# Optimization experiments

Measured on AMD Instinct MI355X. Metric: run time of the kernel, lower is better.

Reference implementation:

```python
import jax, jax.numpy as jnp
import numpy as np


def gcn_conv(x, src, dst, deg_inv_sqrt, W, b, n_nodes):
    # PyG GCNConv: linear transform first, then normalized aggregation (A_hat = D^-1/2 (A+I) D^-1/2)
    h = x @ W                                   # [N, out]
    norm = deg_inv_sqrt[src] * deg_inv_sqrt[dst]  # [E+N]
    msg = h[src] * norm[:, None]                # gather + scale
    out = jax.ops.segment_sum(msg, dst, num_segments=n_nodes)
    return out + b


def setup_inputs() -> dict:
    key = jax.random.key(0)
    ks = jax.random.split(key, 10)
    N, E, D_in, D_h = 50000, 640000, 128, 64
    x = jax.random.normal(ks[0], (N, D_in), dtype=jnp.float32)
    edge_index = jax.random.randint(ks[1], (2, E), 0, N, dtype=jnp.int64)

    def glorot(k, fan_in, fan_out):
        lim = jnp.sqrt(6.0 / (fan_in + fan_out)).astype(jnp.float32)
        return jax.random.uniform(k, (fan_in, fan_out), jnp.float32, -lim, lim)

    return {
        "x": x,
        "edge_index": edge_index,
        "W1": glorot(ks[2], D_in, D_h), "b1": jnp.zeros((D_h,), jnp.float32),
        "W2": glorot(ks[3], D_h, D_h),  "b2": jnp.zeros((D_h,), jnp.float32),
        "W3": glorot(ks[4], D_h, D_h),  "b3": jnp.zeros((D_h,), jnp.float32),
        "W4": glorot(ks[5], D_h, D_in), "b4": jnp.zeros((D_in,), jnp.float32),
    }


def reference(x, edge_index, W1, b1, W2, b2, W3, b3, W4, b4):
    n = x.shape[0]
    loops = jnp.arange(n, dtype=edge_index.dtype)
    src = jnp.concatenate([edge_index[0], loops])  # A + I self-loops
    dst = jnp.concatenate([edge_index[1], loops])
    deg = jax.ops.segment_sum(jnp.ones_like(dst, dtype=x.dtype), dst, num_segments=n)
    deg_inv_sqrt = jnp.where(deg > 0, jax.lax.rsqrt(deg), 0.0)

    h = jax.nn.relu(gcn_conv(x, src, dst, deg_inv_sqrt, W1, b1, n))
    # dropout is identity in eval mode
    z = jax.nn.relu(gcn_conv(h, src, dst, deg_inv_sqrt, W2, b2, n))
    x_hat = jax.nn.relu(gcn_conv(z, src, dst, deg_inv_sqrt, W3, b3, n))
    x_hat = gcn_conv(x_hat, src, dst, deg_inv_sqrt, W4, b4, n)
    return (x_hat, z)
```

## Files before the change

kernel.cpp:

```cpp
#include <hip/hip_runtime.h>
#include <hip/hip_bf16.h>



__global__ __launch_bounds__(256) void init_all(int4* __restrict__ ell4, int nEll4,
                                                int* __restrict__ deg,
                                                int* __restrict__ cursor, int N,
                                                unsigned* __restrict__ gAz,
                                                unsigned* __restrict__ gBz) {
    int i = blockIdx.x * 256 + threadIdx.x;
    if (i < nEll4) ell4[i] = make_int4(N, N, N, N);
    if (i < N) { deg[i] = 0; cursor[i] = 0; }
    if (i < 32) { gAz[i] = 0u; gBz[i] = 0u; }
}

__global__ __launch_bounds__(256) void hist_deg(const int* __restrict__ dst,
                                                int* __restrict__ deg, int E) {
    int e = blockIdx.x * 256 + threadIdx.x;
    if (e < E) atomicAdd(&deg[dst[e]], 1);
}

__global__ __launch_bounds__(256) void dis_k(const int* __restrict__ deg,
                                             float* __restrict__ dis, int N) {
    int i = blockIdx.x * 256 + threadIdx.x;
    if (i < N) dis[i] = rsqrtf((float)(deg[i] + 1));
}

__global__ __launch_bounds__(256) void fill_ell(const int* __restrict__ src,
                                                const int* __restrict__ dst,
                                                int* __restrict__ cursor,
                                                int* __restrict__ ell, int E) {
    int e = blockIdx.x * 256 + threadIdx.x;
    if (e < E) {
        int d = dst[e];
        int slot = atomicAdd(&cursor[d], 1);
        if (slot < 64) ell[(size_t)d * 64 + slot] = src[e];
    }
}


__device__ __forceinline__ ushort r16(float f) {
    __hip_bfloat16 h = __float2bfloat16(f);
    return *reinterpret_cast<ushort*>(&h);
}
__device__ __forceinline__ float bf_lo(unsigned u) {
    return __builtin_bit_cast(float, u << 16);
}
__device__ __forceinline__ float bf_hi(unsigned u) {
    return __builtin_bit_cast(float, u & 0xFFFF0000u);
}

__device__ __forceinline__ void gather_pair_ell(const unsigned* __restrict__ G,
                                                const int* __restrict__ ell,
                                                int n0, int n1c,
                                                int lenA, int lenB, int lane,
                                                float& s0o, float& s1o,
                                                float& s2o, float& s3o) {
    int l32 = lane & 31;
    int idxA = ell[(size_t)n0 * 64 + l32];
    int idxB = ell[(size_t)n1c * 64 + l32];

    int grp     = lane >> 4;
    int p       = grp & 1;
    int nodeSel = grp >> 1;
    int f       = lane & 15;

    int cA = lenA < 32 ? lenA : 32;
    int cB = lenB < 32 ? lenB : 32;
    int cM = cA > cB ? cA : cB;
    int pM = (cM + 1) >> 1;

    float a0 = 0.f, a1 = 0.f, a2 = 0.f, a3 = 0.f;
    float b0 = 0.f, b1 = 0.f, b2 = 0.f, b3 = 0.f;

    for (int k = 0; k < pM; k += 8) {
        uint2 u[8];
#pragma unroll
        for (int i = 0; i < 8; ++i) {
            int e = p + 2 * (k + i);
            int sA = __shfl(idxA, e);
            int sB = __shfl(idxB, e);
            int s = nodeSel ? sB : sA;
            u[i] = *reinterpret_cast<const uint2*>(G + (unsigned)s * 32u + 2 * f);
        }
#pragma unroll
        for (int i = 0; i < 8; ++i) {
            if (i & 1) {
                b0 += bf_lo(u[i].x); b1 += bf_hi(u[i].x);
                b2 += bf_lo(u[i].y); b3 += bf_hi(u[i].y);
            } else {
                a0 += bf_lo(u[i].x); a1 += bf_hi(u[i].x);
                a2 += bf_lo(u[i].y); a3 += bf_hi(u[i].y);
            }
        }
    }
    int nOwn   = nodeSel ? n1c : n0;
    int lenOwn = nodeSel ? lenB : lenA;
    if (lenOwn > 64) lenOwn = 64;
    for (int e2 = 32 + p; e2 < lenOwn; e2 += 2) {
        int s = ell[(size_t)nOwn * 64 + e2];
        uint2 v = *reinterpret_cast<const uint2*>(G + (unsigned)s * 32u + 2 * f);
        a0 += bf_lo(v.x); a1 += bf_hi(v.x);
        a2 += bf_lo(v.y); a3 += bf_hi(v.y);
    }

    float r0 = a0 + b0, r1 = a1 + b1, r2 = a2 + b2, r3 = a3 + b3;
    r0 += __shfl_xor(r0, 16);
    r1 += __shfl_xor(r1, 16);
    r2 += __shfl_xor(r2, 16);
    r3 += __shfl_xor(r3, 16);
    s0o = r0; s1o = r1; s2o = r2; s3o = r3;
}

template <int K, int DOUT>
__global__ __launch_bounds__(256) void gemm_scale(const float* __restrict__ A,
                                                  const float* __restrict__ W,
                                                  const float* __restrict__ dis,
                                                  ushort* __restrict__ G16, int N) {
    constexpr int CG   = DOUT / 4;
    constexpr int RG   = 256 / CG;
    constexpr int ROWS = RG * 4;
    constexpr int LDA  = K + 4;

    __shared__ __align__(16) float a_lds[ROWS * LDA];
    __shared__ __align__(16) float w_lds[K * DOUT];

    int t    = threadIdx.x;
    int row0 = blockIdx.x * ROWS;

    constexpr int WF4 = K * DOUT / 4;
    for (int q = t; q < WF4; q += 256)
        reinterpret_cast<float4*>(w_lds)[q] =
            reinterpret_cast<const float4*>(W)[q];

    constexpr int AF4 = ROWS * K / 4;
    for (int q = t; q < AF4; q += 256) {
        int r  = q / (K / 4);
        int kc = q % (K / 4);
        float4 v = make_float4(0.f, 0.f, 0.f, 0.f);
        int gr = row0 + r;
        if (gr < N)
            v = reinterpret_cast<const float4*>(A + (size_t)gr * K)[kc];
        *reinterpret_cast<float4*>(&a_lds[r * LDA + kc * 4]) = v;
    }
    __syncthreads();

    int c0 = (t % CG) * 4;
    int r0 = (t / CG) * 4;

    float4 acc[4] = {};
#pragma unroll 1
    for (int k = 0; k < K; k += 4) {
        float4 w0 = *reinterpret_cast<const float4*>(&w_lds[(k + 0) * DOUT + c0]);
        float4 w1 = *reinterpret_cast<const float4*>(&w_lds[(k + 1) * DOUT + c0]);
        float4 w2 = *reinterpret_cast<const float4*>(&w_lds[(k + 2) * DOUT + c0]);
        float4 w3 = *reinterpret_cast<const float4*>(&w_lds[(k + 3) * DOUT + c0]);
#pragma unroll
        for (int j = 0; j < 4; ++j) {
            float4 a4 = *reinterpret_cast<const float4*>(&a_lds[(r0 + j) * LDA + k]);
            acc[j].x += a4.x * w0.x + a4.y * w1.x + a4.z * w2.x + a4.w * w3.x;
            acc[j].y += a4.x * w0.y + a4.y * w1.y + a4.z * w2.y + a4.w * w3.y;
            acc[j].z += a4.x * w0.z + a4.y * w1.z + a4.z * w2.z + a4.w * w3.z;
            acc[j].w += a4.x * w0.w + a4.y * w1.w + a4.z * w2.w + a4.w * w3.w;
        }
    }

#pragma unroll
    for (int j = 0; j < 4; ++j) {
        int gr = row0 + r0 + j;
        if (gr < N) {
            float s = dis[gr];
            float4 o = acc[j];
            ushort4 pk;
            pk.x = r16(o.x * s); pk.y = r16(o.y * s);
            pk.z = r16(o.z * s); pk.w = r16(o.w * s);
            *reinterpret_cast<ushort4*>(&G16[(size_t)gr * DOUT + c0]) = pk;
        }
    }
}

template <int K, int DOUT>
__global__ __launch_bounds__(256) void gemm_bias(const float* __restrict__ A,
                                                 const float* __restrict__ W,
                                                 const float* __restrict__ bias,
                                                 float* __restrict__ Out, int N) {
    constexpr int CG   = DOUT / 4;
    constexpr int RG   = 256 / CG;
    constexpr int ROWS = RG * 4;
    constexpr int LDA  = K + 4;

    __shared__ __align__(16) float a_lds[ROWS * LDA];
    __shared__ __align__(16) float w_lds[K * DOUT];

    int t    = threadIdx.x;
    int row0 = blockIdx.x * ROWS;

    constexpr int WF4 = K * DOUT / 4;
    for (int q = t; q < WF4; q += 256)
        reinterpret_cast<float4*>(w_lds)[q] =
            reinterpret_cast<const float4*>(W)[q];

    constexpr int AF4 = ROWS * K / 4;
    for (int q = t; q < AF4; q += 256) {
        int r  = q / (K / 4);
        int kc = q % (K / 4);
        float4 v = make_float4(0.f, 0.f, 0.f, 0.f);
        int gr = row0 + r;
        if (gr < N)
            v = reinterpret_cast<const float4*>(A + (size_t)gr * K)[kc];
        *reinterpret_cast<float4*>(&a_lds[r * LDA + kc * 4]) = v;
    }
    __syncthreads();

    int c0 = (t % CG) * 4;
    int r0 = (t / CG) * 4;

    float4 acc[4] = {};
#pragma unroll 1
    for (int k = 0; k < K; k += 4) {
        float4 w0 = *reinterpret_cast<const float4*>(&w_lds[(k + 0) * DOUT + c0]);
        float4 w1 = *reinterpret_cast<const float4*>(&w_lds[(k + 1) * DOUT + c0]);
        float4 w2 = *reinterpret_cast<const float4*>(&w_lds[(k + 2) * DOUT + c0]);
        float4 w3 = *reinterpret_cast<const float4*>(&w_lds[(k + 3) * DOUT + c0]);
#pragma unroll
        for (int j = 0; j < 4; ++j) {
            float4 a4 = *reinterpret_cast<const float4*>(&a_lds[(r0 + j) * LDA + k]);
            acc[j].x += a4.x * w0.x + a4.y * w1.x + a4.z * w2.x + a4.w * w3.x;
            acc[j].y += a4.x * w0.y + a4.y * w1.y + a4.z * w2.y + a4.w * w3.y;
            acc[j].z += a4.x * w0.z + a4.y * w1.z + a4.z * w2.z + a4.w * w3.z;
            acc[j].w += a4.x * w0.w + a4.y * w1.w + a4.z * w2.w + a4.w * w3.w;
        }
    }

    float4 b4v = *reinterpret_cast<const float4*>(&bias[c0]);
#pragma unroll
    for (int j = 0; j < 4; ++j) {
        int gr = row0 + r0 + j;
        if (gr < N) {
            float4 o = acc[j];
            o.x += b4v.x; o.y += b4v.y; o.z += b4v.z; o.w += b4v.w;
            reinterpret_cast<float4*>(Out + (size_t)gr * DOUT)[c0 / 4] = o;
        }
    }
}

template <bool WRITE_F32>
__global__ __launch_bounds__(256) void agg_gemm_pair(
    const unsigned* __restrict__ G,
    const int* __restrict__ deg,
    const int* __restrict__ ell,
    const float* __restrict__ dis,
    const float* __restrict__ bias,
    const float* __restrict__ Wn,
    unsigned* __restrict__ Gout,
    float* __restrict__ Zout,
    int N) {
    __shared__ __align__(16) float w_lds[64 * 64];
    __shared__ __align__(16) float a_buf[4][2][64];

    int t = threadIdx.x;
    for (int q = t; q < 64 * 64 / 4; q += 256)
        reinterpret_cast<float4*>(w_lds)[q] =
            reinterpret_cast<const float4*>(Wn)[q];
    __syncthreads();

    int wave = t >> 6, lane = t & 63;
    int h = lane >> 5, fl = lane & 31;
    int grp = lane >> 4, f = lane & 15;

    int n0 = (blockIdx.x * 4 + wave) * 2;
    if (n0 >= N) return;
    int n1 = n0 + 1;
    bool hasB = (n1 < N);
    int n1c = hasB ? n1 : n0;
    int nn = h ? n1c : n0;

    int lenA = deg[n0];
    int lenB = hasB ? deg[n1c] : 0;

    float dn0 = dis[n0], dn1 = dis[n1c];
    uint2 us2 = *reinterpret_cast<const uint2*>(G + (size_t)nn * 32 + 2 * f);
    float4 b4 = reinterpret_cast<const float4*>(bias)[f];

    float s0, s1, s2, s3;
    gather_pair_ell(G, ell, n0, n1c, lenA, lenB, lane, s0, s1, s2, s3);

    float dn = h ? dn1 : dn0;
    float v0 = fmaxf(dn * (s0 + bf_lo(us2.x)) + b4.x, 0.f);
    float v1 = fmaxf(dn * (s1 + bf_hi(us2.x)) + b4.y, 0.f);
    float v2 = fmaxf(dn * (s2 + bf_lo(us2.y)) + b4.z, 0.f);
    float v3 = fmaxf(dn * (s3 + bf_hi(us2.y)) + b4.w, 0.f);

    if ((grp & 1) == 0)
        *reinterpret_cast<float4*>(&a_buf[wave][h][4 * f]) =
            make_float4(v0, v1, v2, v3);
    if (WRITE_F32 && (grp == 0 || (grp == 2 && hasB)))
        *reinterpret_cast<float4*>(Zout + (size_t)nn * 64 + 4 * f) =
            make_float4(v0, v1, v2, v3);

    __builtin_amdgcn_wave_barrier();

    float yA0 = 0.f, yA1 = 0.f, yA2 = 0.f, yA3 = 0.f;
    float yB0 = 0.f, yB1 = 0.f, yB2 = 0.f, yB3 = 0.f;
    for (int k = 0; k < 64; k += 4) {
        float4 a4 = *reinterpret_cast<const float4*>(&a_buf[wave][0][k]);
        float4 c4 = *reinterpret_cast<const float4*>(&a_buf[wave][1][k]);
        float w0 = w_lds[(k + 0) * 64 + lane];
        float w1 = w_lds[(k + 1) * 64 + lane];
        float w2 = w_lds[(k + 2) * 64 + lane];
        float w3 = w_lds[(k + 3) * 64 + lane];
        yA0 += a4.x * w0; yA1 += a4.y * w1; yA2 += a4.z * w2; yA3 += a4.w * w3;
        yB0 += c4.x * w0; yB1 += c4.y * w1; yB2 += c4.z * w2; yB3 += c4.w * w3;
    }
    float yA = (yA0 + yA1) + (yA2 + yA3);
    float yB = (yB0 + yB1) + (yB2 + yB3);

    float l0 = __shfl(yA, 2 * fl), h0 = __shfl(yA, 2 * fl + 1);
    float l1 = __shfl(yB, 2 * fl), h1 = __shfl(yB, 2 * fl + 1);
    float yl = h ? l1 : l0;
    float yh = h ? h1 : h0;
    if (h == 0 || hasB) {
        unsigned pk = (unsigned)r16(dn * yl) | ((unsigned)r16(dn * yh) << 16);
        Gout[(unsigned)nn * 32u + fl] = pk;
    }
}

__global__ __launch_bounds__(256) void aggregate_s3(
    const unsigned* __restrict__ G,
    const int* __restrict__ deg,
    const int* __restrict__ ell,
    const float* __restrict__ dis,
    const float* __restrict__ bias,
    unsigned* __restrict__ Out, int N) {
    int t = threadIdx.x;
    int wave = t >> 6, lane = t & 63;
    int h = lane >> 5;
    int grp = lane >> 4, f = lane & 15;

    int n0 = (blockIdx.x * 4 + wave) * 2;
    if (n0 >= N) return;
    int n1 = n0 + 1;
    bool hasB = (n1 < N);
    int n1c = hasB ? n1 : n0;
    int nn = h ? n1c : n0;

    int lenA = deg[n0];
    int lenB = hasB ? deg[n1c] : 0;

    float dn0 = dis[n0], dn1 = dis[n1c];
    uint2 us2 = *reinterpret_cast<const uint2*>(G + (size_t)nn * 32 + 2 * f);
    float4 b4 = reinterpret_cast<const float4*>(bias)[f];

    float s0, s1, s2, s3;
    gather_pair_ell(G, ell, n0, n1c, lenA, lenB, lane, s0, s1, s2, s3);

    float dn = h ? dn1 : dn0;
    float o0 = fmaxf(dn * (s0 + bf_lo(us2.x)) + b4.x, 0.f);
    float o1 = fmaxf(dn * (s1 + bf_hi(us2.x)) + b4.y, 0.f);
    float o2 = fmaxf(dn * (s2 + bf_lo(us2.y)) + b4.z, 0.f);
    float o3 = fmaxf(dn * (s3 + bf_hi(us2.y)) + b4.w, 0.f);

    if (grp == 0 || (grp == 2 && hasB)) {
        uint2 pk2;
        pk2.x = (unsigned)r16(dn * o0) | ((unsigned)r16(dn * o1) << 16);
        pk2.y = (unsigned)r16(dn * o2) | ((unsigned)r16(dn * o3) << 16);
        *reinterpret_cast<uint2*>(Out + (size_t)nn * 32 + 2 * f) = pk2;
    }
}

__global__ __launch_bounds__(256) void aggregate_t(
    const unsigned* __restrict__ G,
    const int* __restrict__ deg,
    const int* __restrict__ ell,
    const float* __restrict__ dis,
    float* __restrict__ Out, int N) {
    int t = threadIdx.x;
    int wave = t >> 6, lane = t & 63;
    int h = lane >> 5;
    int grp = lane >> 4, f = lane & 15;

    int n0 = (blockIdx.x * 4 + wave) * 2;
    if (n0 >= N) return;
    int n1 = n0 + 1;
    bool hasB = (n1 < N);
    int n1c = hasB ? n1 : n0;
    int nn = h ? n1c : n0;

    int lenA = deg[n0];
    int lenB = hasB ? deg[n1c] : 0;

    float dn0 = dis[n0], dn1 = dis[n1c];
    uint2 us2 = *reinterpret_cast<const uint2*>(G + (size_t)nn * 32 + 2 * f);

    float s0, s1, s2, s3;
    gather_pair_ell(G, ell, n0, n1c, lenA, lenB, lane, s0, s1, s2, s3);

    float dn = h ? dn1 : dn0;
    if (grp == 0 || (grp == 2 && hasB))
        *reinterpret_cast<float4*>(Out + (size_t)nn * 64 + 4 * f) =
            make_float4(dn * (s0 + bf_lo(us2.x)), dn * (s1 + bf_hi(us2.x)),
                        dn * (s2 + bf_lo(us2.y)), dn * (s3 + bf_hi(us2.y)));
}


extern "C" void kernel_launch(void* const* d_in, const int* in_sizes, int n_in,
                              void* d_out, int out_size, void* d_ws, size_t ws_size,
                              hipStream_t stream) {
    const float* x     = (const float*)d_in[0];
    const int*   edges = (const int*)d_in[1];
    const float* W1 = (const float*)d_in[2];
    const float* b1 = (const float*)d_in[3];
    const float* W2 = (const float*)d_in[4];
    const float* b2 = (const float*)d_in[5];
    const float* W3 = (const float*)d_in[6];
    const float* b3 = (const float*)d_in[7];
    const float* W4 = (const float*)d_in[8];
    const float* b4 = (const float*)d_in[9];

    const int DIN = 128, DH = 64;
    int N = in_sizes[0] / DIN;
    int E = in_sizes[1] / 2;

    const int* e_src = edges;
    const int* e_dst = edges + E;

    float* out   = (float*)d_out;
    float* x_hat = out;
    float* z     = out + (size_t)N * DIN;

    char*  ws  = (char*)d_ws;
    size_t woff = 0;
    auto carve = [&](size_t bytes) {
        void* p = ws + woff;
        woff = (woff + bytes + 255) & ~(size_t)255;
        return p;
    };
    float*    dis    = (float*)   carve((size_t)N * 4);
    int*      deg    = (int*)     carve((size_t)N * 4);
    int*      cursor = (int*)     carve((size_t)N * 4);
    int*      ell    = (int*)     carve((size_t)N * 64 * 4);
    unsigned* gA     = (unsigned*)carve((size_t)(N + 1) * DH * 2);
    unsigned* gB     = (unsigned*)carve((size_t)(N + 1) * DH * 2);
    float*    tbuf   = (float*)   carve((size_t)N * DH * 4);
    (void)ws_size;

    int nb_e  = (E + 255) / 256;
    int nb_p  = (N + 7) / 8;
    int nEll4 = N * 16;

    init_all<<<(nEll4 + 255) / 256, 256, 0, stream>>>(
        (int4*)ell, nEll4, deg, cursor, N,
        gA + (size_t)N * 32, gB + (size_t)N * 32);
    hist_deg<<<nb_e, 256, 0, stream>>>(e_dst, deg, E);
    dis_k<<<(N + 255) / 256, 256, 0, stream>>>(deg, dis, N);
    fill_ell<<<nb_e, 256, 0, stream>>>(e_src, e_dst, cursor, ell, E);

    gemm_scale<128, 64><<<(N + 63) / 64, 256, 0, stream>>>(
        x, W1, dis, (ushort*)gA, N);

    agg_gemm_pair<false><<<nb_p, 256, 0, stream>>>(
        gA, deg, ell, dis, b1, W2, gB, nullptr, N);

    agg_gemm_pair<true><<<nb_p, 256, 0, stream>>>(
        gB, deg, ell, dis, b2, W3, gA, z, N);

    aggregate_s3<<<nb_p, 256, 0, stream>>>(
        gA, deg, ell, dis, b3, gB, N);

    aggregate_t<<<nb_p, 256, 0, stream>>>(
        gB, deg, ell, dis, tbuf, N);
    gemm_bias<64, 128><<<(N + 31) / 32, 256, 0, stream>>>(tbuf, W4, b4, x_hat, N);
}
```

Measured before the change: 287.8 us.

## Fuse all GCN stages into one cooperative persistent mega-kernel with grid syncs

Replaces the chain of ten separate kernel launches with a single cooperative kernel that runs every phase (ELL init, degree/ELL fill, first GEMM, four aggregation layers, final GEMM) in grid-stride loops separated by grid.sync(). The degree histogram and ELL fill are merged into one edge pass, and dis is computed inside the first GEMM. The GEMMs now read activations straight from global memory instead of staging them in LDS. The aim is to remove launch overhead and inter-kernel gaps, at the cost of grid-wide barriers, a grid limited by occupancy, and less latency hiding in the phases that use persistent loops.

New measurement: 724.1 us. +151.6%, slower.

```diff
diff --git a/kernel.cpp b/kernel.cpp
--- a/kernel.cpp
+++ b/kernel.cpp
@@ -1,42 +1,9 @@
 #include <hip/hip_runtime.h>
 #include <hip/hip_bf16.h>
-
-
-
-__global__ __launch_bounds__(256) void init_all(int4* __restrict__ ell4, int nEll4,
-                                                int* __restrict__ deg,
-                                                int* __restrict__ cursor, int N,
-                                                unsigned* __restrict__ gAz,
-                                                unsigned* __restrict__ gBz) {
-    int i = blockIdx.x * 256 + threadIdx.x;
-    if (i < nEll4) ell4[i] = make_int4(N, N, N, N);
-    if (i < N) { deg[i] = 0; cursor[i] = 0; }
-    if (i < 32) { gAz[i] = 0u; gBz[i] = 0u; }
-}
-
-__global__ __launch_bounds__(256) void hist_deg(const int* __restrict__ dst,
-                                                int* __restrict__ deg, int E) {
-    int e = blockIdx.x * 256 + threadIdx.x;
-    if (e < E) atomicAdd(&deg[dst[e]], 1);
-}
-
-__global__ __launch_bounds__(256) void dis_k(const int* __restrict__ deg,
-                                             float* __restrict__ dis, int N) {
-    int i = blockIdx.x * 256 + threadIdx.x;
-    if (i < N) dis[i] = rsqrtf((float)(deg[i] + 1));
-}
-
-__global__ __launch_bounds__(256) void fill_ell(const int* __restrict__ src,
-                                                const int* __restrict__ dst,
-                                                int* __restrict__ cursor,
-                                                int* __restrict__ ell, int E) {
-    int e = blockIdx.x * 256 + threadIdx.x;
-    if (e < E) {
-        int d = dst[e];
-        int slot = atomicAdd(&cursor[d], 1);
-        if (slot < 64) ell[(size_t)d * 64 + slot] = src[e];
-    }
-}
+#include <hip/hip_cooperative_groups.h>
+
+namespace cg = cooperative_groups;
+
 
 
 __device__ __forceinline__ ushort r16(float f) {
@@ -112,154 +79,16 @@
     s0o = r0; s1o = r1; s2o = r2; s3o = r3;
 }
 
-template <int K, int DOUT>
-__global__ __launch_bounds__(256) void gemm_scale(const float* __restrict__ A,
-                                                  const float* __restrict__ W,
-                                                  const float* __restrict__ dis,
-                                                  ushort* __restrict__ G16, int N) {
-    constexpr int CG   = DOUT / 4;
-    constexpr int RG   = 256 / CG;
-    constexpr int ROWS = RG * 4;
-    constexpr int LDA  = K + 4;
-
-    __shared__ __align__(16) float a_lds[ROWS * LDA];
-    __shared__ __align__(16) float w_lds[K * DOUT];
-
-    int t    = threadIdx.x;
-    int row0 = blockIdx.x * ROWS;
-
-    constexpr int WF4 = K * DOUT / 4;
-    for (int q = t; q < WF4; q += 256)
-        reinterpret_cast<float4*>(w_lds)[q] =
-            reinterpret_cast<const float4*>(W)[q];
-
-    constexpr int AF4 = ROWS * K / 4;
-    for (int q = t; q < AF4; q += 256) {
-        int r  = q / (K / 4);
-        int kc = q % (K / 4);
-        float4 v = make_float4(0.f, 0.f, 0.f, 0.f);
-        int gr = row0 + r;
-        if (gr < N)
-            v = reinterpret_cast<const float4*>(A + (size_t)gr * K)[kc];
-        *reinterpret_cast<float4*>(&a_lds[r * LDA + kc * 4]) = v;
-    }
+template <bool WRITE_Z>
+__device__ __forceinline__ void agg_fused_phase(
+    const unsigned* __restrict__ G, const int* __restrict__ deg,
+    const int* __restrict__ ell, const float* __restrict__ dis,
+    const float* __restrict__ bias, const float* __restrict__ Wn,
+    unsigned* __restrict__ Gout, float* __restrict__ Zout, int N,
+    float* w_lds, float (*a_buf)[2][64]) {
+    int t = threadIdx.x;
     __syncthreads();
-
-    int c0 = (t % CG) * 4;
-    int r0 = (t / CG) * 4;
-
-    float4 acc[4] = {};
-#pragma unroll 1
-    for (int k = 0; k < K; k += 4) {
-        float4 w0 = *reinterpret_cast<const float4*>(&w_lds[(k + 0) * DOUT + c0]);
-        float4 w1 = *reinterpret_cast<const float4*>(&w_lds[(k + 1) * DOUT + c0]);
-        float4 w2 = *reinterpret_cast<const float4*>(&w_lds[(k + 2) * DOUT + c0]);
-        float4 w3 = *reinterpret_cast<const float4*>(&w_lds[(k + 3) * DOUT + c0]);
-#pragma unroll
-        for (int j = 0; j < 4; ++j) {
-            float4 a4 = *reinterpret_cast<const float4*>(&a_lds[(r0 + j) * LDA + k]);
-            acc[j].x += a4.x * w0.x + a4.y * w1.x + a4.z * w2.x + a4.w * w3.x;
-            acc[j].y += a4.x * w0.y + a4.y * w1.y + a4.z * w2.y + a4.w * w3.y;
-            acc[j].z += a4.x * w0.z + a4.y * w1.z + a4.z * w2.z + a4.w * w3.z;
-            acc[j].w += a4.x * w0.w + a4.y * w1.w + a4.z * w2.w + a4.w * w3.w;
-        }
-    }
-
-#pragma unroll
-    for (int j = 0; j < 4; ++j) {
-        int gr = row0 + r0 + j;
-        if (gr < N) {
-            float s = dis[gr];
-            float4 o = acc[j];
-            ushort4 pk;
-            pk.x = r16(o.x * s); pk.y = r16(o.y * s);
-            pk.z = r16(o.z * s); pk.w = r16(o.w * s);
-            *reinterpret_cast<ushort4*>(&G16[(size_t)gr * DOUT + c0]) = pk;
-        }
-    }
-}
-
-template <int K, int DOUT>
-__global__ __launch_bounds__(256) void gemm_bias(const float* __restrict__ A,
-                                                 const float* __restrict__ W,
-                                                 const float* __restrict__ bias,
-                                                 float* __restrict__ Out, int N) {
-    constexpr int CG   = DOUT / 4;
-    constexpr int RG   = 256 / CG;
-    constexpr int ROWS = RG * 4;
-    constexpr int LDA  = K + 4;
-
-    __shared__ __align__(16) float a_lds[ROWS * LDA];
-    __shared__ __align__(16) float w_lds[K * DOUT];
-
-    int t    = threadIdx.x;
-    int row0 = blockIdx.x * ROWS;
-
-    constexpr int WF4 = K * DOUT / 4;
-    for (int q = t; q < WF4; q += 256)
-        reinterpret_cast<float4*>(w_lds)[q] =
-            reinterpret_cast<const float4*>(W)[q];
-
-    constexpr int AF4 = ROWS * K / 4;
-    for (int q = t; q < AF4; q += 256) {
-        int r  = q / (K / 4);
-        int kc = q % (K / 4);
-        float4 v = make_float4(0.f, 0.f, 0.f, 0.f);
-        int gr = row0 + r;
-        if (gr < N)
-            v = reinterpret_cast<const float4*>(A + (size_t)gr * K)[kc];
-        *reinterpret_cast<float4*>(&a_lds[r * LDA + kc * 4]) = v;
-    }
-    __syncthreads();
-
-    int c0 = (t % CG) * 4;
-    int r0 = (t / CG) * 4;
-
-    float4 acc[4] = {};
-#pragma unroll 1
-    for (int k = 0; k < K; k += 4) {
-        float4 w0 = *reinterpret_cast<const float4*>(&w_lds[(k + 0) * DOUT + c0]);
-        float4 w1 = *reinterpret_cast<const float4*>(&w_lds[(k + 1) * DOUT + c0]);
-        float4 w2 = *reinterpret_cast<const float4*>(&w_lds[(k + 2) * DOUT + c0]);
-        float4 w3 = *reinterpret_cast<const float4*>(&w_lds[(k + 3) * DOUT + c0]);
-#pragma unroll
-        for (int j = 0; j < 4; ++j) {
-            float4 a4 = *reinterpret_cast<const float4*>(&a_lds[(r0 + j) * LDA + k]);
-            acc[j].x += a4.x * w0.x + a4.y * w1.x + a4.z * w2.x + a4.w * w3.x;
-            acc[j].y += a4.x * w0.y + a4.y * w1.y + a4.z * w2.y + a4.w * w3.y;
-            acc[j].z += a4.x * w0.z + a4.y * w1.z + a4.z * w2.z + a4.w * w3.z;
-            acc[j].w += a4.x * w0.w + a4.y * w1.w + a4.z * w2.w + a4.w * w3.w;
-        }
-    }
-
-    float4 b4v = *reinterpret_cast<const float4*>(&bias[c0]);
-#pragma unroll
-    for (int j = 0; j < 4; ++j) {
-        int gr = row0 + r0 + j;
-        if (gr < N) {
-            float4 o = acc[j];
-            o.x += b4v.x; o.y += b4v.y; o.z += b4v.z; o.w += b4v.w;
-            reinterpret_cast<float4*>(Out + (size_t)gr * DOUT)[c0 / 4] = o;
-        }
-    }
-}
-
-template <bool WRITE_F32>
-__global__ __launch_bounds__(256) void agg_gemm_pair(
-    const unsigned* __restrict__ G,
-    const int* __restrict__ deg,
-    const int* __restrict__ ell,
-    const float* __restrict__ dis,
-    const float* __restrict__ bias,
-    const float* __restrict__ Wn,
-    unsigned* __restrict__ Gout,
-    float* __restrict__ Zout,
-    int N) {
-    __shared__ __align__(16) float w_lds[64 * 64];
-    __shared__ __align__(16) float a_buf[4][2][64];
-
-    int t = threadIdx.x;
-    for (int q = t; q < 64 * 64 / 4; q += 256)
+    for (int q = t; q < 1024; q += 256)
         reinterpret_cast<float4*>(w_lds)[q] =
             reinterpret_cast<const float4*>(Wn)[q];
     __syncthreads();
@@ -267,139 +96,293 @@
     int wave = t >> 6, lane = t & 63;
     int h = lane >> 5, fl = lane & 31;
     int grp = lane >> 4, f = lane & 15;
-
-    int n0 = (blockIdx.x * 4 + wave) * 2;
-    if (n0 >= N) return;
-    int n1 = n0 + 1;
-    bool hasB = (n1 < N);
-    int n1c = hasB ? n1 : n0;
-    int nn = h ? n1c : n0;
-
-    int lenA = deg[n0];
-    int lenB = hasB ? deg[n1c] : 0;
-
-    float dn0 = dis[n0], dn1 = dis[n1c];
-    uint2 us2 = *reinterpret_cast<const uint2*>(G + (size_t)nn * 32 + 2 * f);
-    float4 b4 = reinterpret_cast<const float4*>(bias)[f];
-
-    float s0, s1, s2, s3;
-    gather_pair_ell(G, ell, n0, n1c, lenA, lenB, lane, s0, s1, s2, s3);
-
-    float dn = h ? dn1 : dn0;
-    float v0 = fmaxf(dn * (s0 + bf_lo(us2.x)) + b4.x, 0.f);
-    float v1 = fmaxf(dn * (s1 + bf_hi(us2.x)) + b4.y, 0.f);
-    float v2 = fmaxf(dn * (s2 + bf_lo(us2.y)) + b4.z, 0.f);
-    float v3 = fmaxf(dn * (s3 + bf_hi(us2.y)) + b4.w, 0.f);
-
-    if ((grp & 1) == 0)
-        *reinterpret_cast<float4*>(&a_buf[wave][h][4 * f]) =
-            make_float4(v0, v1, v2, v3);
-    if (WRITE_F32 && (grp == 0 || (grp == 2 && hasB)))
-        *reinterpret_cast<float4*>(Zout + (size_t)nn * 64 + 4 * f) =
-            make_float4(v0, v1, v2, v3);
-
-    __builtin_amdgcn_wave_barrier();
-
-    float yA0 = 0.f, yA1 = 0.f, yA2 = 0.f, yA3 = 0.f;
-    float yB0 = 0.f, yB1 = 0.f, yB2 = 0.f, yB3 = 0.f;
-    for (int k = 0; k < 64; k += 4) {
-        float4 a4 = *reinterpret_cast<const float4*>(&a_buf[wave][0][k]);
-        float4 c4 = *reinterpret_cast<const float4*>(&a_buf[wave][1][k]);
-        float w0 = w_lds[(k + 0) * 64 + lane];
-        float w1 = w_lds[(k + 1) * 64 + lane];
-        float w2 = w_lds[(k + 2) * 64 + lane];
-        float w3 = w_lds[(k + 3) * 64 + lane];
-        yA0 += a4.x * w0; yA1 += a4.y * w1; yA2 += a4.z * w2; yA3 += a4.w * w3;
-        yB0 += c4.x * w0; yB1 += c4.y * w1; yB2 += c4.z * w2; yB3 += c4.w * w3;
-    }
-    float yA = (yA0 + yA1) + (yA2 + yA3);
-    float yB = (yB0 + yB1) + (yB2 + yB3);
-
-    float l0 = __shfl(yA, 2 * fl), h0 = __shfl(yA, 2 * fl + 1);
-    float l1 = __shfl(yB, 2 * fl), h1 = __shfl(yB, 2 * fl + 1);
-    float yl = h ? l1 : l0;
-    float yh = h ? h1 : h0;
-    if (h == 0 || hasB) {
-        unsigned pk = (unsigned)r16(dn * yl) | ((unsigned)r16(dn * yh) << 16);
-        Gout[(unsigned)nn * 32u + fl] = pk;
-    }
-}
-
-__global__ __launch_bounds__(256) void aggregate_s3(
-    const unsigned* __restrict__ G,
-    const int* __restrict__ deg,
-    const int* __restrict__ ell,
-    const float* __restrict__ dis,
-    const float* __restrict__ bias,
-    unsigned* __restrict__ Out, int N) {
+    int nPB = (N + 7) / 8;
+
+    for (int pb = blockIdx.x; pb < nPB; pb += gridDim.x) {
+        int n0 = (pb * 4 + wave) * 2;
+        if (n0 < N) {
+            int n1 = n0 + 1;
+            bool hasB = (n1 < N);
+            int n1c = hasB ? n1 : n0;
+            int nn = h ? n1c : n0;
+
+            int lenA = deg[n0];
+            int lenB = hasB ? deg[n1c] : 0;
+
+            float dn0 = dis[n0], dn1 = dis[n1c];
+            uint2 us2 = *reinterpret_cast<const uint2*>(G + (size_t)nn * 32 + 2 * f);
+            float4 b4v = reinterpret_cast<const float4*>(bias)[f];
+
+            float s0, s1, s2, s3;
+            gather_pair_ell(G, ell, n0, n1c, lenA, lenB, lane, s0, s1, s2, s3);
+
+            float dn = h ? dn1 : dn0;
+            float v0 = fmaxf(dn * (s0 + bf_lo(us2.x)) + b4v.x, 0.f);
+            float v1 = fmaxf(dn * (s1 + bf_hi(us2.x)) + b4v.y, 0.f);
+            float v2 = fmaxf(dn * (s2 + bf_lo(us2.y)) + b4v.z, 0.f);
+            float v3 = fmaxf(dn * (s3 + bf_hi(us2.y)) + b4v.w, 0.f);
+
+            if ((grp & 1) == 0)
+                *reinterpret_cast<float4*>(&a_buf[wave][h][4 * f]) =
+                    make_float4(v0, v1, v2, v3);
+            if (WRITE_Z && (grp == 0 || (grp == 2 && hasB)))
+                *reinterpret_cast<float4*>(Zout + (size_t)nn * 64 + 4 * f) =
+                    make_float4(v0, v1, v2, v3);
+
+            __builtin_amdgcn_wave_barrier();
+
+            float yA0 = 0.f, yA1 = 0.f, yA2 = 0.f, yA3 = 0.f;
+            float yB0 = 0.f, yB1 = 0.f, yB2 = 0.f, yB3 = 0.f;
+            for (int k = 0; k < 64; k += 4) {
+                float4 a4 = *reinterpret_cast<const float4*>(&a_buf[wave][0][k]);
+                float4 c4 = *reinterpret_cast<const float4*>(&a_buf[wave][1][k]);
+                float w0 = w_lds[(k + 0) * 64 + lane];
+                float w1 = w_lds[(k + 1) * 64 + lane];
+                float w2 = w_lds[(k + 2) * 64 + lane];
+                float w3 = w_lds[(k + 3) * 64 + lane];
+                yA0 += a4.x * w0; yA1 += a4.y * w1; yA2 += a4.z * w2; yA3 += a4.w * w3;
+                yB0 += c4.x * w0; yB1 += c4.y * w1; yB2 += c4.z * w2; yB3 += c4.w * w3;
+            }
+            float yA = (yA0 + yA1) + (yA2 + yA3);
+            float yB = (yB0 + yB1) + (yB2 + yB3);
+
+            float l0 = __shfl(yA, 2 * fl), hv0 = __shfl(yA, 2 * fl + 1);
+            float l1 = __shfl(yB, 2 * fl), hv1 = __shfl(yB, 2 * fl + 1);
+            float yl = h ? l1 : l0;
+            float yh = h ? hv1 : hv0;
+            if (h == 0 || hasB) {
+                unsigned pk = (unsigned)r16(dn * yl) | ((unsigned)r16(dn * yh) << 16);
+                Gout[(unsigned)nn * 32u + fl] = pk;
+            }
+            __builtin_amdgcn_wave_barrier();
+        }
+    }
+}
+
+__device__ __forceinline__ void agg_s3_phase(
+    const unsigned* __restrict__ G, const int* __restrict__ deg,
+    const int* __restrict__ ell, const float* __restrict__ dis,
+    const float* __restrict__ bias, unsigned* __restrict__ Out, int N) {
     int t = threadIdx.x;
     int wave = t >> 6, lane = t & 63;
-    int h = lane >> 5;
-    int grp = lane >> 4, f = lane & 15;
-
-    int n0 = (blockIdx.x * 4 + wave) * 2;
-    if (n0 >= N) return;
-    int n1 = n0 + 1;
-    bool hasB = (n1 < N);
-    int n1c = hasB ? n1 : n0;
-    int nn = h ? n1c : n0;
-
-    int lenA = deg[n0];
-    int lenB = hasB ? deg[n1c] : 0;
-
-    float dn0 = dis[n0], dn1 = dis[n1c];
-    uint2 us2 = *reinterpret_cast<const uint2*>(G + (size_t)nn * 32 + 2 * f);
-    float4 b4 = reinterpret_cast<const float4*>(bias)[f];
-
-    float s0, s1, s2, s3;
-    gather_pair_ell(G, ell, n0, n1c, lenA, lenB, lane, s0, s1, s2, s3);
-
-    float dn = h ? dn1 : dn0;
-    float o0 = fmaxf(dn * (s0 + bf_lo(us2.x)) + b4.x, 0.f);
-    float o1 = fmaxf(dn * (s1 + bf_hi(us2.x)) + b4.y, 0.f);
-    float o2 = fmaxf(dn * (s2 + bf_lo(us2.y)) + b4.z, 0.f);
-    float o3 = fmaxf(dn * (s3 + bf_hi(us2.y)) + b4.w, 0.f);
-
-    if (grp == 0 || (grp == 2 && hasB)) {
-        uint2 pk2;
-        pk2.x = (unsigned)r16(dn * o0) | ((unsigned)r16(dn * o1) << 16);
-        pk2.y = (unsigned)r16(dn * o2) | ((unsigned)r16(dn * o3) << 16);
-        *reinterpret_cast<uint2*>(Out + (size_t)nn * 32 + 2 * f) = pk2;
-    }
-}
-
-__global__ __launch_bounds__(256) void aggregate_t(
-    const unsigned* __restrict__ G,
-    const int* __restrict__ deg,
-    const int* __restrict__ ell,
-    const float* __restrict__ dis,
+    int h = lane >> 5, grp = lane >> 4, f = lane & 15;
+    int nPB = (N + 7) / 8;
+
+    for (int pb = blockIdx.x; pb < nPB; pb += gridDim.x) {
+        int n0 = (pb * 4 + wave) * 2;
+        if (n0 >= N) continue;
+        int n1 = n0 + 1;
+        bool hasB = (n1 < N);
+        int n1c = hasB ? n1 : n0;
+        int nn = h ? n1c : n0;
+
+        int lenA = deg[n0];
+        int lenB = hasB ? deg[n1c] : 0;
+
+        float dn0 = dis[n0], dn1 = dis[n1c];
+        uint2 us2 = *reinterpret_cast<const uint2*>(G + (size_t)nn * 32 + 2 * f);
+        float4 b4v = reinterpret_cast<const float4*>(bias)[f];
+
+        float s0, s1, s2, s3;
+        gather_pair_ell(G, ell, n0, n1c, lenA, lenB, lane, s0, s1, s2, s3);
+
+        float dn = h ? dn1 : dn0;
+        float o0 = fmaxf(dn * (s0 + bf_lo(us2.x)) + b4v.x, 0.f);
+        float o1 = fmaxf(dn * (s1 + bf_hi(us2.x)) + b4v.y, 0.f);
+        float o2 = fmaxf(dn * (s2 + bf_lo(us2.y)) + b4v.z, 0.f);
+        float o3 = fmaxf(dn * (s3 + bf_hi(us2.y)) + b4v.w, 0.f);
+
+        if (grp == 0 || (grp == 2 && hasB)) {
+            uint2 pk2;
+            pk2.x = (unsigned)r16(dn * o0) | ((unsigned)r16(dn * o1) << 16);
+            pk2.y = (unsigned)r16(dn * o2) | ((unsigned)r16(dn * o3) << 16);
+            *reinterpret_cast<uint2*>(Out + (size_t)nn * 32 + 2 * f) = pk2;
+        }
+    }
+}
+
+__device__ __forceinline__ void agg_t_phase(
+    const unsigned* __restrict__ G, const int* __restrict__ deg,
+    const int* __restrict__ ell, const float* __restrict__ dis,
     float* __restrict__ Out, int N) {
     int t = threadIdx.x;
     int wave = t >> 6, lane = t & 63;
-    int h = lane >> 5;
-    int grp = lane >> 4, f = lane & 15;
-
-    int n0 = (blockIdx.x * 4 + wave) * 2;
-    if (n0 >= N) return;
-    int n1 = n0 + 1;
-    bool hasB = (n1 < N);
-    int n1c = hasB ? n1 : n0;
-    int nn = h ? n1c : n0;
-
-    int lenA = deg[n0];
-    int lenB = hasB ? deg[n1c] : 0;
-
-    float dn0 = dis[n0], dn1 = dis[n1c];
-    uint2 us2 = *reinterpret_cast<const uint2*>(G + (size_t)nn * 32 + 2 * f);
-
-    float s0, s1, s2, s3;
-    gather_pair_ell(G, ell, n0, n1c, lenA, lenB, lane, s0, s1, s2, s3);
-
-    float dn = h ? dn1 : dn0;
-    if (grp == 0 || (grp == 2 && hasB))
-        *reinterpret_cast<float4*>(Out + (size_t)nn * 64 + 4 * f) =
-            make_float4(dn * (s0 + bf_lo(us2.x)), dn * (s1 + bf_hi(us2.x)),
-                        dn * (s2 + bf_lo(us2.y)), dn * (s3 + bf_hi(us2.y)));
+    int h = lane >> 5, grp = lane >> 4, f = lane & 15;
+    int nPB = (N + 7) / 8;
+
+    for (int pb = blockIdx.x; pb < nPB; pb += gridDim.x) {
+        int n0 = (pb * 4 + wave) * 2;
+        if (n0 >= N) continue;
+        int n1 = n0 + 1;
+        bool hasB = (n1 < N);
+        int n1c = hasB ? n1 : n0;
+        int nn = h ? n1c : n0;
+
+        int lenA = deg[n0];
+        int lenB = hasB ? deg[n1c] : 0;
+
+        float dn0 = dis[n0], dn1 = dis[n1c];
+        uint2 us2 = *reinterpret_cast<const uint2*>(G + (size_t)nn * 32 + 2 * f);
+
+        float s0, s1, s2, s3;
+        gather_pair_ell(G, ell, n0, n1c, lenA, lenB, lane, s0, s1, s2, s3);
+
+        float dn = h ? dn1 : dn0;
+        if (grp == 0 || (grp == 2 && hasB))
+            *reinterpret_cast<float4*>(Out + (size_t)nn * 64 + 4 * f) =
+                make_float4(dn * (s0 + bf_lo(us2.x)), dn * (s1 + bf_hi(us2.x)),
+                            dn * (s2 + bf_lo(us2.y)), dn * (s3 + bf_hi(us2.y)));
+    }
+}
+
+__global__ __launch_bounds__(256) void mega_kernel(
+    const float* __restrict__ x,
+    const int* __restrict__ e_src, const int* __restrict__ e_dst,
+    const float* __restrict__ W1, const float* __restrict__ b1,
+    const float* __restrict__ W2, const float* __restrict__ b2,
+    const float* __restrict__ W3, const float* __restrict__ b3,
+    const float* __restrict__ W4, const float* __restrict__ b4,
+    float* __restrict__ dis, int* __restrict__ deg, int* __restrict__ cursor,
+    int* __restrict__ ell, unsigned* __restrict__ gA, unsigned* __restrict__ gB,
+    float* __restrict__ tbuf, float* __restrict__ x_hat, float* __restrict__ z,
+    int N, int E) {
+    __shared__ __align__(16) float w_lds[64 * 64];
+    __shared__ __align__(16) float a_buf[4][2][64];
+    cg::grid_group grid = cg::this_grid();
+
+    const int tid  = threadIdx.x;
+    const int gtid = blockIdx.x * 256 + tid;
+    const int gstr = gridDim.x * 256;
+
+    {
+        int nEll4 = N * 16;
+        int4* ell4 = reinterpret_cast<int4*>(ell);
+        int4 fv = make_int4(N, N, N, N);
+        for (int i = gtid; i < nEll4; i += gstr) ell4[i] = fv;
+        for (int i = gtid; i < N; i += gstr) { deg[i] = 0; cursor[i] = 0; }
+        unsigned* gAz = gA + (size_t)N * 32;
+        unsigned* gBz = gB + (size_t)N * 32;
+        for (int i = gtid; i < 32; i += gstr) { gAz[i] = 0u; gBz[i] = 0u; }
+    }
+    grid.sync();
+
+    for (int e = gtid; e < E; e += gstr) {
+        int d = e_dst[e];
+        atomicAdd(&deg[d], 1);
+        int slot = atomicAdd(&cursor[d], 1);
+        if (slot < 64) ell[(size_t)d * 64 + slot] = e_src[e];
+    }
+    grid.sync();
+
+    {
+        int c0 = (tid & 15) * 4;
+        int r0 = (tid >> 4) * 4;
+        int nbl = (N + 63) / 64;
+        for (int bl = blockIdx.x; bl < nbl; bl += gridDim.x) {
+            int row0 = bl * 64;
+            float4 acc[4] = {};
+            for (int half = 0; half < 2; ++half) {
+                __syncthreads();
+                const float4* Wf4 = reinterpret_cast<const float4*>(W1) + half * 1024;
+                for (int q = tid; q < 1024; q += 256)
+                    reinterpret_cast<float4*>(w_lds)[q] = Wf4[q];
+                __syncthreads();
+#pragma unroll 1
+                for (int k = 0; k < 64; k += 4) {
+                    float4 w0 = *reinterpret_cast<const float4*>(&w_lds[(k + 0) * 64 + c0]);
+                    float4 w1 = *reinterpret_cast<const float4*>(&w_lds[(k + 1) * 64 + c0]);
+                    float4 w2 = *reinterpret_cast<const float4*>(&w_lds[(k + 2) * 64 + c0]);
+                    float4 w3 = *reinterpret_cast<const float4*>(&w_lds[(k + 3) * 64 + c0]);
+#pragma unroll
+                    for (int j = 0; j < 4; ++j) {
+                        int gr = row0 + r0 + j;
+                        int grc = gr < N ? gr : N - 1;
+                        float4 a4 = *reinterpret_cast<const float4*>(
+                            x + (size_t)grc * 128 + half * 64 + k);
+                        acc[j].x += a4.x * w0.x + a4.y * w1.x + a4.z * w2.x + a4.w * w3.x;
+                        acc[j].y += a4.x * w0.y + a4.y * w1.y + a4.z * w2.y + a4.w * w3.y;
+                        acc[j].z += a4.x * w0.z + a4.y * w1.z + a4.z * w2.z + a4.w * w3.z;
+                        acc[j].w += a4.x * w0.w + a4.y * w1.w + a4.z * w2.w + a4.w * w3.w;
+                    }
+                }
+            }
+            ushort* g16 = reinterpret_cast<ushort*>(gA);
+#pragma unroll
+            for (int j = 0; j < 4; ++j) {
+                int gr = row0 + r0 + j;
+                if (gr < N) {
+                    float dn = rsqrtf((float)(deg[gr] + 1));
+                    if (c0 == 0) dis[gr] = dn;
+                    float4 o = acc[j];
+                    ushort4 pk;
+                    pk.x = r16(o.x * dn); pk.y = r16(o.y * dn);
+                    pk.z = r16(o.z * dn); pk.w = r16(o.w * dn);
+                    *reinterpret_cast<ushort4*>(&g16[(size_t)gr * 64 + c0]) = pk;
+                }
+            }
+        }
+    }
+    grid.sync();
+
+    agg_fused_phase<false>(gA, deg, ell, dis, b1, W2, gB, nullptr, N, w_lds, a_buf);
+    grid.sync();
+
+    agg_fused_phase<true>(gB, deg, ell, dis, b2, W3, gA, z, N, w_lds, a_buf);
+    grid.sync();
+
+    agg_s3_phase(gA, deg, ell, dis, b3, gB, N);
+    grid.sync();
+
+    agg_t_phase(gB, deg, ell, dis, tbuf, N);
+    grid.sync();
+
+    {
+        int c0 = (tid & 15) * 4;
+        int r0 = (tid >> 4) * 4;
+        int nbl = (N + 63) / 64;
+        for (int bl = blockIdx.x; bl < nbl; bl += gridDim.x) {
+            int row0 = bl * 64;
+            for (int hc = 0; hc < 2; ++hc) {
+                __syncthreads();
+                for (int q = tid; q < 1024; q += 256) {
+                    int k = q >> 4, ci = q & 15;
+                    reinterpret_cast<float4*>(w_lds)[q] =
+                        reinterpret_cast<const float4*>(W4)[k * 32 + hc * 16 + ci];
+                }
+                __syncthreads();
+                float4 acc[4] = {};
+#pragma unroll 1
+                for (int k = 0; k < 64; k += 4) {
+                    float4 w0 = *reinterpret_cast<const float4*>(&w_lds[(k + 0) * 64 + c0]);
+                    float4 w1 = *reinterpret_cast<const float4*>(&w_lds[(k + 1) * 64 + c0]);
+                    float4 w2 = *reinterpret_cast<const float4*>(&w_lds[(k + 2) * 64 + c0]);
+                    float4 w3 = *reinterpret_cast<const float4*>(&w_lds[(k + 3) * 64 + c0]);
+#pragma unroll
+                    for (int j = 0; j < 4; ++j) {
+                        int gr = row0 + r0 + j;
+                        int grc = gr < N ? gr : N - 1;
+                        float4 a4 = *reinterpret_cast<const float4*>(
+                            tbuf + (size_t)grc * 64 + k);
+                        acc[j].x += a4.x * w0.x + a4.y * w1.x + a4.z * w2.x + a4.w * w3.x;
+                        acc[j].y += a4.x * w0.y + a4.y * w1.y + a4.z * w2.y + a4.w * w3.y;
+                        acc[j].z += a4.x * w0.z + a4.y * w1.z + a4.z * w2.z + a4.w * w3.z;
+                        acc[j].w += a4.x * w0.w + a4.y * w1.w + a4.z * w2.w + a4.w * w3.w;
+                    }
+                }
+                float4 bb = *reinterpret_cast<const float4*>(b4 + hc * 64 + c0);
+#pragma unroll
+                for (int j = 0; j < 4; ++j) {
+                    int gr = row0 + r0 + j;
+                    if (gr < N) {
+                        float4 o = acc[j];
+                        o.x += bb.x; o.y += bb.y; o.z += bb.z; o.w += bb.w;
+                        *reinterpret_cast<float4*>(
+                            x_hat + (size_t)gr * 128 + hc * 64 + c0) = o;
+                    }
+                }
+            }
+        }
+    }
 }
 
 
@@ -444,30 +427,30 @@
     float*    tbuf   = (float*)   carve((size_t)N * DH * 4);
     (void)ws_size;
 
-    int nb_e  = (E + 255) / 256;
-    int nb_p  = (N + 7) / 8;
-    int nEll4 = N * 16;
-
-    init_all<<<(nEll4 + 255) / 256, 256, 0, stream>>>(
-        (int4*)ell, nEll4, deg, cursor, N,
-        gA + (size_t)N * 32, gB + (size_t)N * 32);
-    hist_deg<<<nb_e, 256, 0, stream>>>(e_dst, deg, E);
-    dis_k<<<(N + 255) / 256, 256, 0, stream>>>(deg, dis, N);
-    fill_ell<<<nb_e, 256, 0, stream>>>(e_src, e_dst, cursor, ell, E);
-
-    gemm_scale<128, 64><<<(N + 63) / 64, 256, 0, stream>>>(
-        x, W1, dis, (ushort*)gA, N);
-
-    agg_gemm_pair<false><<<nb_p, 256, 0, stream>>>(
-        gA, deg, ell, dis, b1, W2, gB, nullptr, N);
-
-    agg_gemm_pair<true><<<nb_p, 256, 0, stream>>>(
-        gB, deg, ell, dis, b2, W3, gA, z, N);
-
-    aggregate_s3<<<nb_p, 256, 0, stream>>>(
-        gA, deg, ell, dis, b3, gB, N);
-
-    aggregate_t<<<nb_p, 256, 0, stream>>>(
-        gB, deg, ell, dis, tbuf, N);
-    gemm_bias<64, 128><<<(N + 31) / 32, 256, 0, stream>>>(tbuf, W4, b4, x_hat, N);
-}
+    static int coopBlocks = 0;
+    if (coopBlocks == 0) {
+        int perCU = 0;
+        hipOccupancyMaxActiveBlocksPerMultiprocessor(&perCU, mega_kernel, 256, 0);
+        if (perCU <= 0) perCU = 4;
+        hipDeviceProp_t prop{};
+        int dev = 0;
+        hipGetDevice(&dev);
+        hipGetDeviceProperties(&prop, dev);
+        int cus = prop.multiProcessorCount > 0 ? prop.multiProcessorCount : 256;
+        coopBlocks = perCU * cus;
+    }
+    int work = (N + 7) / 8;
+    int grid = coopBlocks < work ? coopBlocks : work;
+    if (grid < 1) grid = 1;
+
+    void* kargs[] = {
+        (void*)&x, (void*)&e_src, (void*)&e_dst,
+        (void*)&W1, (void*)&b1, (void*)&W2, (void*)&b2,
+        (void*)&W3, (void*)&b3, (void*)&W4, (void*)&b4,
+        (void*)&dis, (void*)&deg, (void*)&cursor, (void*)&ell,
+        (void*)&gA, (void*)&gB, (void*)&tbuf,
+        (void*)&x_hat, (void*)&z, (void*)&N, (void*)&E,
+    };
+    hipLaunchCooperativeKernel((void*)mega_kernel, dim3(grid), dim3(256),
+                               kargs, 0, stream);
+}
```
